# Optimization experiments

Hardware: AMD Instinct MI355X
Metric: run time of the kernel (lower is better)

## Reference

```python
import jax, jax.numpy as jnp
import numpy as np

N, FIN, F, H = 4096, 128, 64, 8
NEG = -1e10


def setup_inputs() -> dict:
    key = jax.random.key(0)
    ks = jax.random.split(key, 6)
    X = jax.random.normal(ks[0], (N, FIN), dtype=jnp.float32)
    # sparse-ish binary adjacency with self loops, stored dense (as the layer expects)
    A = (jax.random.uniform(ks[1], (N, N)) < 0.05).astype(jnp.int32)
    A = A.at[jnp.arange(N), jnp.arange(N)].set(1)
    W = jax.random.normal(ks[2], (H, FIN, F), dtype=jnp.float32) * (1.0 / np.sqrt(FIN))
    b = jnp.zeros((H, F), dtype=jnp.float32)
    a_self = jax.random.normal(ks[3], (H, F), dtype=jnp.float32) * (1.0 / np.sqrt(F))
    a_neigh = jax.random.normal(ks[4], (H, F), dtype=jnp.float32) * (1.0 / np.sqrt(F))
    return {"X": X, "A": A, "W": W, "b": b, "a_self": a_self, "a_neigh": a_neigh}


def reference(X, A, W, b, a_self, a_neigh):
    # Dropout layers run in inference mode in the original call -> identity.
    feats = jnp.einsum('nf,hfo->hno', X, W)              # [H, N, F]
    s_self = jnp.einsum('hno,ho->hn', feats, a_self)     # [H, N]
    s_neigh = jnp.einsum('hno,ho->hn', feats, a_neigh)   # [H, N]
    scores = s_self[:, :, None] + s_neigh[:, None, :]    # [H, N, N]
    scores = jnp.where(scores > 0, scores, 0.2 * scores)  # LeakyReLU(0.2)
    mask = (1.0 - A.astype(jnp.float32)) * NEG            # [N, N]
    attn = jax.nn.softmax(scores + mask[None], axis=-1)   # [H, N, N]
    out = jnp.einsum('hnm,hmo->hno', attn, feats) + b[:, None, :]
    out = jax.nn.elu(out)                                 # [H, N, F]
    # concat heads -> [N, H*F]
    return jnp.transpose(out, (1, 0, 2)).reshape(N, H * F)
```

## Files before the change

kernel.cpp:

```cpp
#include <hip/hip_runtime.h>
#include <cmath>


#define NN 4096
#define FIN 128
#define FF 64
#define HH 8

typedef _Float16 h2 __attribute__((ext_vector_type(2)));
typedef _Float16 h4 __attribute__((ext_vector_type(4)));
typedef _Float16 h8 __attribute__((ext_vector_type(8)));
typedef float f32x2 __attribute__((ext_vector_type(2)));
typedef float f32x4 __attribute__((ext_vector_type(4)));

union H8 {
  h8 v;
  h2 p[4];
};
union H4 {
  h4 v;
  h2 p[2];
};

__global__ __launch_bounds__(256) void pack_kernel(
    const int* __restrict__ A, const float* __restrict__ W,
    const float* __restrict__ X, unsigned long long* __restrict__ bits,
    _Float16* __restrict__ Wsw, _Float16* __restrict__ Xsw) {
  const int b = blockIdx.x;
  const int tid = threadIdx.x;
  const int wave = tid >> 6, lane = tid & 63;
  if (b < NN) {
    __shared__ int ldsT[4][4][256];
    const int* ar = A + (size_t)b * NN;
    int4 v[4];
#pragma unroll
    for (int it = 0; it < 4; ++it) {
      const int g = wave * 4 + it;
      v[it] = *(const int4*)(ar + g * 256 + lane * 4);
    }
#pragma unroll
    for (int it = 0; it < 4; ++it) *(int4*)&ldsT[wave][it][lane * 4] = v[it];
    unsigned long long* br = bits + ((size_t)b << 6);
#pragma unroll
    for (int it = 0; it < 4; ++it) {
      const int g = wave * 4 + it;
      int w0 = ldsT[wave][it][0 * 64 + lane];
      int w1 = ldsT[wave][it][1 * 64 + lane];
      int w2 = ldsT[wave][it][2 * 64 + lane];
      int w3 = ldsT[wave][it][3 * 64 + lane];
      unsigned long long m0 = __ballot(w0 != 0);
      unsigned long long m1 = __ballot(w1 != 0);
      unsigned long long m2 = __ballot(w2 != 0);
      unsigned long long m3 = __ballot(w3 != 0);
      if (lane == 0) {
        ulonglong2 p0 = {m0, m1}, p1 = {m2, m3};
        *(ulonglong2*)(br + g * 4 + 0) = p0;
        *(ulonglong2*)(br + g * 4 + 2) = p1;
      }
    }
  } else if (b < NN + 2) {
    const int h0 = (b - NN) * 4;
    for (int h = h0; h < h0 + 4; ++h) {
      for (int c = tid; c < 1024; c += 256) {
        int ln = c & 63, nb = (c >> 6) & 3, kt = c >> 8;
        int f = nb * 16 + (ln & 15);
        int k0 = kt * 32 + (ln >> 4) * 8;
        h8 v;
#pragma unroll
        for (int j = 0; j < 8; ++j)
          v[j] = (_Float16)W[((size_t)(h * FIN) + k0 + j) * FF + f];
        *(h8*)(Wsw + ((size_t)(((h * 4 + kt) * 4 + nb) * 64 + ln)) * 8) = v;
      }
    }
  } else {
    const int tile = (b - NN - 2) * 4 + wave;
    const int l16 = lane & 15, quad = lane >> 4;
    const float* xr = X + (size_t)(tile * 16 + l16) * FIN;
#pragma unroll
    for (int kt = 0; kt < 4; ++kt) {
      int k0 = kt * 32 + quad * 8;
      f32x4 x0 = *(const f32x4*)(xr + k0);
      f32x4 x1 = *(const f32x4*)(xr + k0 + 4);
      h8 v = {(_Float16)x0[0], (_Float16)x0[1], (_Float16)x0[2],
              (_Float16)x0[3], (_Float16)x1[0], (_Float16)x1[1],
              (_Float16)x1[2], (_Float16)x1[3]};
      *(h8*)(Xsw + ((size_t)((tile * 4 + kt) * 64 + lane)) * 8) = v;
    }
  }
}

__global__ __launch_bounds__(256) void feats_kernel(
    const _Float16* __restrict__ Xsw, const _Float16* __restrict__ Wsw,
    const float* __restrict__ a_self, const float* __restrict__ a_neigh,
    _Float16* __restrict__ feats_sw, _Float16* __restrict__ es_h,
    _Float16* __restrict__ esn_h, _Float16* __restrict__ et_h,
    _Float16* __restrict__ etn_h) {
  const int h = blockIdx.y;
  const int tid = threadIdx.x, wave = tid >> 6, lane = tid & 63;
  const int l16 = lane & 15, quad = lane >> 4;
  const int rt = blockIdx.x * 4 + wave;
  const int r0 = rt * 16;

  f32x4 acc[4];
#pragma unroll
  for (int nb = 0; nb < 4; ++nb) acc[nb] = (f32x4){0.f, 0.f, 0.f, 0.f};

  const _Float16* xp = Xsw + ((size_t)(rt * 4) * 64 + lane) * 8;
  const _Float16* wp = Wsw + ((size_t)(h * 16) * 64 + lane) * 8;
  h8 Af[4];
#pragma unroll
  for (int kt = 0; kt < 4; ++kt) Af[kt] = *(const h8*)(xp + kt * 512);
#pragma unroll
  for (int kt = 0; kt < 4; ++kt)
#pragma unroll
    for (int nb = 0; nb < 4; ++nb) {
      h8 Bf = *(const h8*)(wp + (kt * 4 + nb) * 512);
      acc[nb] = __builtin_amdgcn_mfma_f32_16x16x32_f16(Af[kt], Bf, acc[nb], 0, 0, 0);
    }

  float as[4], an[4];
#pragma unroll
  for (int nb = 0; nb < 4; ++nb) {
    as[nb] = a_self[h * FF + nb * 16 + l16];
    an[nb] = a_neigh[h * FF + nb * 16 + l16];
  }
#pragma unroll
  for (int r = 0; r < 4; ++r) {
    float ps = acc[0][r] * as[0] + acc[1][r] * as[1] + acc[2][r] * as[2] +
               acc[3][r] * as[3];
    float pn = acc[0][r] * an[0] + acc[1][r] * an[1] + acc[2][r] * an[2] +
               acc[3][r] * an[3];
#pragma unroll
    for (int m = 1; m <= 8; m <<= 1) {
      ps += __shfl_xor(ps, m, 64);
      pn += __shfl_xor(pn, m, 64);
    }
    if (l16 == 0) {
      int node = h * NN + r0 + quad * 4 + r;
      es_h[node] = (_Float16)__expf(ps - 2.0f);
      esn_h[node] = (_Float16)__expf(0.2f * ps - 2.0f);
      et_h[node] = (_Float16)__expf(pn - 2.0f);
      etn_h[node] = (_Float16)__expf(0.2f * pn - 2.0f);
    }
  }

  const int kb = r0 >> 5;
  const int quadA = ((r0 >> 4) & 1) * 2 + (quad >> 1);
  const int jbase = (quad & 1) << 2;
#pragma unroll
  for (int nb = 0; nb < 4; ++nb) {
    h4 v = {(_Float16)acc[nb][0], (_Float16)acc[nb][1], (_Float16)acc[nb][2],
            (_Float16)acc[nb][3]};
    size_t off = ((size_t)((h * 128 + kb) * 4 + nb) << 9) +
                 ((quadA * 16 + l16) << 3) + jbase;
    *(h4*)(feats_sw + off) = v;
  }
}

__global__ __launch_bounds__(256, 4) void attn_kernel(
    const unsigned long long* __restrict__ Abits,
    const _Float16* __restrict__ feats_sw, const _Float16* __restrict__ es_h,
    const _Float16* __restrict__ esn_h, const _Float16* __restrict__ et_h,
    const _Float16* __restrict__ etn_h, const float* __restrict__ bias,
    float* __restrict__ out) {
  const int bid = blockIdx.x;
  const int h = bid & 7, n0 = (bid >> 3) << 5;
  const int tid = threadIdx.x, wave = tid >> 6, lane = tid & 63;
  const int l16 = lane & 15, quad = lane >> 4;

  __shared__ h4 lut16[16];
  __shared__ float accL[4][16][66];
  __shared__ float denL[4][32];
  if (tid < 16) {
    h4 m;
#pragma unroll
    for (int j = 0; j < 4; ++j) m[j] = (_Float16)((tid >> j) & 1);
    lut16[tid] = m;
  }
  __syncthreads();

  h2 esp[2], esnp[2];
#pragma unroll
  for (int rg = 0; rg < 2; ++rg) {
    _Float16 e = es_h[h * NN + n0 + rg * 16 + l16];
    _Float16 en = esn_h[h * NN + n0 + rg * 16 + l16];
    esp[rg] = (h2){e, e};
    esnp[rg] = (h2){en, en};
  }

  f32x4 acc[2][4];
  f32x4 accd[2];
#pragma unroll
  for (int rg = 0; rg < 2; ++rg) {
    accd[rg] = (f32x4){0.f, 0.f, 0.f, 0.f};
#pragma unroll
    for (int nb = 0; nb < 4; ++nb) acc[rg][nb] = (f32x4){0.f, 0.f, 0.f, 0.f};
  }
  const h8 onesB = {(_Float16)1.f, (_Float16)1.f, (_Float16)1.f,
                    (_Float16)1.f, (_Float16)1.f, (_Float16)1.f,
                    (_Float16)1.f, (_Float16)1.f};

  const uint2* ab = (const uint2*)Abits;
  const int rowbase = n0 + l16;
  const _Float16* etp = et_h + h * NN + (quad << 3);
  const _Float16* etnp = etn_h + h * NN + (quad << 3);
  const _Float16* fb = feats_sw + ((size_t)h << 18) + (lane << 3);

#pragma unroll 2
  for (int ct = wave; ct < 64; ct += 4) {
    uint2 bits[2];
#pragma unroll
    for (int rg = 0; rg < 2; ++rg)
      bits[rg] = ab[((rowbase + rg * 16) << 6) + ct];
    const _Float16* fbt = fb + (ct << 12);
#pragma unroll
    for (int kf = 0; kf < 2; ++kf) {
      H8 ET, ETN;
      ET.v = *(const h8*)(etp + (ct << 6) + kf * 32);
      ETN.v = *(const h8*)(etnp + (ct << 6) + kf * 32);
      const _Float16* fk = fbt + (kf << 11);
      h8 B0 = *(const h8*)(fk);
      h8 B1 = *(const h8*)(fk + 512);
      h8 B2 = *(const h8*)(fk + 1024);
      h8 B3 = *(const h8*)(fk + 1536);
#pragma unroll
      for (int rg = 0; rg < 2; ++rg) {
        unsigned word = kf ? bits[rg].y : bits[rg].x;
        unsigned byt = (word >> (quad << 3)) & 0xFFu;
        H4 mlo, mhi;
        mlo.v = lut16[byt & 15u];
        mhi.v = lut16[byt >> 4];
        H8 P;
#pragma unroll
        for (int p = 0; p < 4; ++p) {
          h2 a = esp[rg] * ET.p[p];
          h2 b = esnp[rg] * ETN.p[p];
          h2 r = __builtin_elementwise_max(a, b);
          P.p[p] = r * (p < 2 ? mlo.p[p] : mhi.p[p - 2]);
        }
        acc[rg][0] =
            __builtin_amdgcn_mfma_f32_16x16x32_f16(P.v, B0, acc[rg][0], 0, 0, 0);
        acc[rg][1] =
            __builtin_amdgcn_mfma_f32_16x16x32_f16(P.v, B1, acc[rg][1], 0, 0, 0);
        acc[rg][2] =
            __builtin_amdgcn_mfma_f32_16x16x32_f16(P.v, B2, acc[rg][2], 0, 0, 0);
        acc[rg][3] =
            __builtin_amdgcn_mfma_f32_16x16x32_f16(P.v, B3, acc[rg][3], 0, 0, 0);
        accd[rg] =
            __builtin_amdgcn_mfma_f32_16x16x32_f16(P.v, onesB, accd[rg], 0, 0, 0);
      }
    }
  }

  if (l16 == 0) {
#pragma unroll
    for (int rg = 0; rg < 2; ++rg)
#pragma unroll
      for (int r = 0; r < 4; ++r)
        denL[wave][rg * 16 + quad * 4 + r] = accd[rg][r];
  }

  const int erow = tid >> 4, ec0 = (tid & 15) << 2;
#pragma unroll
  for (int ph = 0; ph < 2; ++ph) {
    __syncthreads();
#pragma unroll
    for (int nb = 0; nb < 4; ++nb)
#pragma unroll
      for (int r = 0; r < 4; ++r)
        accL[wave][quad * 4 + r][nb * 16 + l16] = acc[ph][nb][r];
    __syncthreads();
    const int grow = ph * 16 + erow;
    float dn = denL[0][grow] + denL[1][grow] + denL[2][grow] + denL[3][grow];
    float inv = 1.0f / dn;
    f32x2 v0 = (f32x2){0.f, 0.f}, v1 = (f32x2){0.f, 0.f};
#pragma unroll
    for (int w = 0; w < 4; ++w) {
      v0 += *(const f32x2*)&accL[w][erow][ec0];
      v1 += *(const f32x2*)&accL[w][erow][ec0 + 2];
    }
    const f32x4 bv = *(const f32x4*)(bias + h * FF + ec0);
    f32x4 v = {v0[0], v0[1], v1[0], v1[1]};
#pragma unroll
    for (int i = 0; i < 4; ++i) {
      float x = v[i] * inv + bv[i];
      v[i] = x > 0.f ? x : (__expf(x) - 1.0f);
    }
    *(f32x4*)(out + (size_t)(n0 + grow) * (HH * FF) + h * FF + ec0) = v;
  }
}

extern "C" void kernel_launch(void* const* d_in, const int* in_sizes, int n_in,
                              void* d_out, int out_size, void* d_ws,
                              size_t ws_size, hipStream_t stream) {
  const float* X = (const float*)d_in[0];
  const int* A = (const int*)d_in[1];
  const float* W = (const float*)d_in[2];
  const float* b = (const float*)d_in[3];
  const float* a_self = (const float*)d_in[4];
  const float* a_neigh = (const float*)d_in[5];
  float* out = (float*)d_out;

  char* ws = (char*)d_ws;
  unsigned long long* Abits = (unsigned long long*)ws;
  _Float16* feats_sw = (_Float16*)(ws + (2u << 20));
  _Float16* es_h = (_Float16*)(ws + (6u << 20));
  _Float16* esn_h = (_Float16*)(ws + (6u << 20) + (64u << 10));
  _Float16* et_h = (_Float16*)(ws + (6u << 20) + (128u << 10));
  _Float16* etn_h = (_Float16*)(ws + (6u << 20) + (192u << 10));
  _Float16* Wsw = (_Float16*)(ws + (6u << 20) + (256u << 10));
  _Float16* Xsw = (_Float16*)(ws + (6u << 20) + (384u << 10));

  pack_kernel<<<NN + 66, 256, 0, stream>>>(A, W, X, Abits, Wsw, Xsw);
  feats_kernel<<<dim3(64, 8), 256, 0, stream>>>(Xsw, Wsw, a_self, a_neigh,
                                                feats_sw, es_h, esn_h, et_h,
                                                etn_h);
  attn_kernel<<<1024, 256, 0, stream>>>(Abits, feats_sw, es_h, esn_h, et_h,
                                        etn_h, b, out);
}
```

Baseline: 154.4 us.

## Prefetch next column tile in registers and transpose adjacency bitmask for coalesced reads

The attention loop is rewritten as a software pipeline. Each iteration issues global loads for the next column tile (mask bits, exp factors, feature fragments) into registers before running the MFMAs on the current tile, so memory latency is hidden behind compute. The pack kernel also writes a column-major copy of the adjacency bitmask, which lets the 16 lanes of a row group read consecutive 64-bit words. The extra registers this needs force launch bounds down from 4 to 3 blocks per SM, and the pack kernel now does scattered 8-byte stores for the transposed copy.

Result: slower. 167.5 us (+8.5%).

```diff
diff --git a/kernel.cpp b/kernel.cpp
--- a/kernel.cpp
+++ b/kernel.cpp
@@ -25,7 +25,8 @@
 __global__ __launch_bounds__(256) void pack_kernel(
     const int* __restrict__ A, const float* __restrict__ W,
     const float* __restrict__ X, unsigned long long* __restrict__ bits,
-    _Float16* __restrict__ Wsw, _Float16* __restrict__ Xsw) {
+    unsigned long long* __restrict__ bitsT, _Float16* __restrict__ Wsw,
+    _Float16* __restrict__ Xsw) {
   const int b = blockIdx.x;
   const int tid = threadIdx.x;
   const int wave = tid >> 6, lane = tid & 63;
@@ -56,6 +57,10 @@
         ulonglong2 p0 = {m0, m1}, p1 = {m2, m3};
         *(ulonglong2*)(br + g * 4 + 0) = p0;
         *(ulonglong2*)(br + g * 4 + 2) = p1;
+        bitsT[(size_t)(g * 4 + 0) * NN + b] = m0;
+        bitsT[(size_t)(g * 4 + 1) * NN + b] = m1;
+        bitsT[(size_t)(g * 4 + 2) * NN + b] = m2;
+        bitsT[(size_t)(g * 4 + 3) * NN + b] = m3;
       }
     }
   } else if (b < NN + 2) {
@@ -157,8 +162,37 @@
   }
 }
 
-__global__ __launch_bounds__(256, 4) void attn_kernel(
-    const unsigned long long* __restrict__ Abits,
+struct CtD {
+  uint2 b0, b1;
+  h8 ET0, ETN0, ET1, ETN1;
+  h8 B0[4], B1[4];
+};
+
+static __device__ __forceinline__ CtD load_ct(
+    const unsigned long long* __restrict__ btp,
+    const _Float16* __restrict__ etp, const _Float16* __restrict__ etnp,
+    const _Float16* __restrict__ fb, int ct, int rowbase) {
+  CtD s;
+  const unsigned long long* bp = btp + (size_t)ct * NN + rowbase;
+  s.b0 = *(const uint2*)(bp);
+  s.b1 = *(const uint2*)(bp + 16);
+  const _Float16* e = etp + (ct << 6);
+  const _Float16* en = etnp + (ct << 6);
+  s.ET0 = *(const h8*)(e);
+  s.ET1 = *(const h8*)(e + 32);
+  s.ETN0 = *(const h8*)(en);
+  s.ETN1 = *(const h8*)(en + 32);
+  const _Float16* fk = fb + ((size_t)ct << 12);
+#pragma unroll
+  for (int nb = 0; nb < 4; ++nb) {
+    s.B0[nb] = *(const h8*)(fk + nb * 512);
+    s.B1[nb] = *(const h8*)(fk + 2048 + nb * 512);
+  }
+  return s;
+}
+
+__global__ __launch_bounds__(256, 3) void attn_kernel(
+    const unsigned long long* __restrict__ bitsT,
     const _Float16* __restrict__ feats_sw, const _Float16* __restrict__ es_h,
     const _Float16* __restrict__ esn_h, const _Float16* __restrict__ et_h,
     const _Float16* __restrict__ etn_h, const float* __restrict__ bias,
@@ -200,32 +234,26 @@
                     (_Float16)1.f, (_Float16)1.f, (_Float16)1.f,
                     (_Float16)1.f, (_Float16)1.f};
 
-  const uint2* ab = (const uint2*)Abits;
   const int rowbase = n0 + l16;
   const _Float16* etp = et_h + h * NN + (quad << 3);
   const _Float16* etnp = etn_h + h * NN + (quad << 3);
   const _Float16* fb = feats_sw + ((size_t)h << 18) + (lane << 3);
 
-#pragma unroll 2
-  for (int ct = wave; ct < 64; ct += 4) {
-    uint2 bits[2];
-#pragma unroll
-    for (int rg = 0; rg < 2; ++rg)
-      bits[rg] = ab[((rowbase + rg * 16) << 6) + ct];
-    const _Float16* fbt = fb + (ct << 12);
+  CtD cur = load_ct(bitsT, etp, etnp, fb, wave, rowbase);
+
+#pragma unroll 1
+  for (int i = 0; i < 16; ++i) {
+    CtD nxt;
+    if (i < 15) nxt = load_ct(bitsT, etp, etnp, fb, wave + (i + 1) * 4, rowbase);
 #pragma unroll
     for (int kf = 0; kf < 2; ++kf) {
-      H8 ET, ETN;
-      ET.v = *(const h8*)(etp + (ct << 6) + kf * 32);
-      ETN.v = *(const h8*)(etnp + (ct << 6) + kf * 32);
-      const _Float16* fk = fbt + (kf << 11);
-      h8 B0 = *(const h8*)(fk);
-      h8 B1 = *(const h8*)(fk + 512);
-      h8 B2 = *(const h8*)(fk + 1024);
-      h8 B3 = *(const h8*)(fk + 1536);
+      const H8 ET = {kf ? cur.ET1 : cur.ET0};
+      const H8 ETN = {kf ? cur.ETN1 : cur.ETN0};
+      const h8* B = kf ? cur.B1 : cur.B0;
 #pragma unroll
       for (int rg = 0; rg < 2; ++rg) {
-        unsigned word = kf ? bits[rg].y : bits[rg].x;
+        const uint2 bb = rg ? cur.b1 : cur.b0;
+        unsigned word = kf ? bb.y : bb.x;
         unsigned byt = (word >> (quad << 3)) & 0xFFu;
         H4 mlo, mhi;
         mlo.v = lut16[byt & 15u];
@@ -239,17 +267,18 @@
           P.p[p] = r * (p < 2 ? mlo.p[p] : mhi.p[p - 2]);
         }
         acc[rg][0] =
-            __builtin_amdgcn_mfma_f32_16x16x32_f16(P.v, B0, acc[rg][0], 0, 0, 0);
+            __builtin_amdgcn_mfma_f32_16x16x32_f16(P.v, B[0], acc[rg][0], 0, 0, 0);
         acc[rg][1] =
-            __builtin_amdgcn_mfma_f32_16x16x32_f16(P.v, B1, acc[rg][1], 0, 0, 0);
+            __builtin_amdgcn_mfma_f32_16x16x32_f16(P.v, B[1], acc[rg][1], 0, 0, 0);
         acc[rg][2] =
-            __builtin_amdgcn_mfma_f32_16x16x32_f16(P.v, B2, acc[rg][2], 0, 0, 0);
+            __builtin_amdgcn_mfma_f32_16x16x32_f16(P.v, B[2], acc[rg][2], 0, 0, 0);
         acc[rg][3] =
-            __builtin_amdgcn_mfma_f32_16x16x32_f16(P.v, B3, acc[rg][3], 0, 0, 0);
+            __builtin_amdgcn_mfma_f32_16x16x32_f16(P.v, B[3], acc[rg][3], 0, 0, 0);
         accd[rg] =
             __builtin_amdgcn_mfma_f32_16x16x32_f16(P.v, onesB, accd[rg], 0, 0, 0);
       }
     }
+    cur = nxt;
   }
 
   if (l16 == 0) {
@@ -303,18 +332,19 @@
 
   char* ws = (char*)d_ws;
   unsigned long long* Abits = (unsigned long long*)ws;
-  _Float16* feats_sw = (_Float16*)(ws + (2u << 20));
-  _Float16* es_h = (_Float16*)(ws + (6u << 20));
-  _Float16* esn_h = (_Float16*)(ws + (6u << 20) + (64u << 10));
-  _Float16* et_h = (_Float16*)(ws + (6u << 20) + (128u << 10));
-  _Float16* etn_h = (_Float16*)(ws + (6u << 20) + (192u << 10));
-  _Float16* Wsw = (_Float16*)(ws + (6u << 20) + (256u << 10));
-  _Float16* Xsw = (_Float16*)(ws + (6u << 20) + (384u << 10));
-
-  pack_kernel<<<NN + 66, 256, 0, stream>>>(A, W, X, Abits, Wsw, Xsw);
+  unsigned long long* bitsT = (unsigned long long*)(ws + (2u << 20));
+  _Float16* feats_sw = (_Float16*)(ws + (4u << 20));
+  _Float16* es_h = (_Float16*)(ws + (8u << 20));
+  _Float16* esn_h = (_Float16*)(ws + (8u << 20) + (64u << 10));
+  _Float16* et_h = (_Float16*)(ws + (8u << 20) + (128u << 10));
+  _Float16* etn_h = (_Float16*)(ws + (8u << 20) + (192u << 10));
+  _Float16* Wsw = (_Float16*)(ws + (8u << 20) + (256u << 10));
+  _Float16* Xsw = (_Float16*)(ws + (8u << 20) + (384u << 10));
+
+  pack_kernel<<<NN + 66, 256, 0, stream>>>(A, W, X, Abits, bitsT, Wsw, Xsw);
   feats_kernel<<<dim3(64, 8), 256, 0, stream>>>(Xsw, Wsw, a_self, a_neigh,
                                                 feats_sw, es_h, esn_h, et_h,
                                                 etn_h);
-  attn_kernel<<<1024, 256, 0, stream>>>(Abits, feats_sw, es_h, esn_h, et_h,
+  attn_kernel<<<1024, 256, 0, stream>>>(bitsT, feats_sw, es_h, esn_h, et_h,
                                         etn_h, b, out);
 }
```
